# Kernel tuning notes

Measured on AMD Instinct MI355X. Metric: run time of the kernel, lower is better.

Reference implementation:

```python
import jax, jax.numpy as jnp
import numpy as np

EPS = 1e-5

def _layernorm(x, w, b):
    mu = jnp.mean(x, axis=-1, keepdims=True)
    var = jnp.mean(jnp.square(x - mu), axis=-1, keepdims=True)
    return (x - mu) * jax.lax.rsqrt(var + EPS) * w + b

def setup_inputs() -> dict:
    key = jax.random.key(0)
    ks = jax.random.split(key, 9)
    N, P_DIM, D = 16384, 3072, 1024
    patches = jax.random.normal(ks[0], (N, P_DIM), dtype=jnp.float32)
    bbox_coords = jax.random.uniform(ks[1], (N, 4), dtype=jnp.float32)
    ln1_w = jnp.ones((P_DIM,), dtype=jnp.float32)
    ln1_b = jnp.zeros((P_DIM,), dtype=jnp.float32)
    W_patch = jax.random.normal(ks[2], (D, P_DIM), dtype=jnp.float32) * (P_DIM ** -0.5)
    class_emb = jax.random.normal(ks[3], (1, 1, D), dtype=jnp.float32)
    W_pos = jax.random.normal(ks[4], (D, 4), dtype=jnp.float32) * 0.5
    b_pos = jax.random.normal(ks[5], (D,), dtype=jnp.float32) * 0.02
    class_pos = jax.random.normal(ks[6], (1, D), dtype=jnp.float32)
    return {"patches": patches, "bbox_coords": bbox_coords, "ln1_w": ln1_w,
            "ln1_b": ln1_b, "W_patch": W_patch, "class_emb": class_emb,
            "W_pos": W_pos, "b_pos": b_pos, "class_pos": class_pos}

def reference(patches, bbox_coords, ln1_w, ln1_b, W_patch, class_emb, W_pos, b_pos, class_pos):
    # Batched equivalent of the per-patch loop: LayerNorm -> Linear (no bias).
    # NOTE: torch code computes patch_norm2 but appends the PRE-norm2 embedding,
    # so norm2 is dead code and omitted here.
    x = _layernorm(patches, ln1_w, ln1_b)                      # [N, patch_dim]
    patch_embeds = jnp.einsum('np,dp->nd', x, W_patch)          # [N, D]
    embeddings = jnp.concatenate([class_emb, patch_embeds[None]], axis=1)  # [1, N+1, D]
    pos = jnp.einsum('nc,dc->nd', bbox_coords, W_pos) + b_pos   # [N, D]
    pos_full = jnp.concatenate([class_pos[None], pos[None]], axis=1)       # [1, N+1, D]
    return embeddings + pos_full
```

## Files before the change

kernel.cpp:

```cpp
#include <hip/hip_runtime.h>

typedef unsigned short u16;
typedef __attribute__((ext_vector_type(8))) short bf16x8;
typedef __attribute__((ext_vector_type(4))) float f32x4;

#define AS1C(p) ((const __attribute__((address_space(1))) void*)(p))
#define AS3(p)  ((__attribute__((address_space(3))) void*)(p))

__device__ __forceinline__ u16 f2bf(float f) {
    unsigned u = __float_as_uint(f);
    u += 0x7fffu + ((u >> 16) & 1u);
    return (u16)(u >> 16);
}

__global__ __launch_bounds__(256) void ln_cast_kernel(
    const float* __restrict__ x, const float* __restrict__ w,
    const float* __restrict__ b, u16* __restrict__ A, int K)
{
    const int row = blockIdx.x;
    const int t = threadIdx.x;
    const float* xr = x + (size_t)row * K;

    float4 v[3];
#pragma unroll
    for (int i = 0; i < 3; ++i)
        v[i] = *(const float4*)&xr[(i * 256 + t) * 4];

    float s = 0.f;
#pragma unroll
    for (int i = 0; i < 3; ++i) s += v[i].x + v[i].y + v[i].z + v[i].w;
#pragma unroll
    for (int off = 32; off; off >>= 1) s += __shfl_down(s, off);

    __shared__ float red[8];
    const int wid = t >> 6, lane = t & 63;
    if (lane == 0) red[wid] = s;
    __syncthreads();
    const float mu = (red[0] + red[1] + red[2] + red[3]) * (1.0f / 3072.0f);

    float sq = 0.f;
#pragma unroll
    for (int i = 0; i < 3; ++i) {
        float dx = v[i].x - mu, dy = v[i].y - mu, dz = v[i].z - mu, dw = v[i].w - mu;
        sq += dx * dx + dy * dy + dz * dz + dw * dw;
    }
#pragma unroll
    for (int off = 32; off; off >>= 1) sq += __shfl_down(sq, off);
    if (lane == 0) red[4 + wid] = sq;
    __syncthreads();
    const float var = (red[4] + red[5] + red[6] + red[7]) * (1.0f / 3072.0f);
    const float inv = rsqrtf(var + 1e-5f);

#pragma unroll
    for (int i = 0; i < 3; ++i) {
        const int j = (i * 256 + t) * 4;
        const float4 wv = *(const float4*)&w[j];
        const float4 bv = *(const float4*)&b[j];
        ushort4 o;
        o.x = f2bf((v[i].x - mu) * inv * wv.x + bv.x);
        o.y = f2bf((v[i].y - mu) * inv * wv.y + bv.y);
        o.z = f2bf((v[i].z - mu) * inv * wv.z + bv.z);
        o.w = f2bf((v[i].w - mu) * inv * wv.w + bv.w);
        *(ushort4*)&A[(size_t)row * K + j] = o;
    }
}

__global__ __launch_bounds__(256) void cast_w_kernel(
    const float* __restrict__ Wp, u16* __restrict__ Wb, int n4)
{
    const int i = blockIdx.x * 256 + threadIdx.x;
    if (i < n4) {
        const float4 v = ((const float4*)Wp)[i];
        ushort4 o;
        o.x = f2bf(v.x); o.y = f2bf(v.y); o.z = f2bf(v.z); o.w = f2bf(v.w);
        ((ushort4*)Wb)[i] = o;
    }
}

__global__ __launch_bounds__(256) void class_row_kernel(
    const float* __restrict__ ce, const float* __restrict__ cp,
    float* __restrict__ out, int D)
{
    const int i = blockIdx.x * 256 + threadIdx.x;
    if (i < D) out[i] = ce[i] + cp[i];
}

#define STG_A(BUFOFS, R0, T_) \
    __builtin_amdgcn_global_load_lds(AS1C(aS + (size_t)(R0) * 3072 + (T_) * 64), \
                                     AS3(dA + (BUFOFS) + (R0) * 128), 16, 0, 0)
#define STG_B(BUFOFS, R0, T_) \
    __builtin_amdgcn_global_load_lds(AS1C(bS + (size_t)(R0) * 3072 + (T_) * 64), \
                                     AS3(dB + (BUFOFS) + (R0) * 128), 16, 0, 0)

#define MFMA(d, a, b) d = __builtin_amdgcn_mfma_f32_16x16x32_bf16(a, b, d, 0, 0, 0)

#define PHASE(BUF, MH, CK, STG, WT) do {                                          \
    const char* Lb = L + (BUF);                                                   \
    bf16x8 a0 = *(const bf16x8*)(Lb + aRowBase + (MH)*8192 + 0*2048 + (CK));      \
    bf16x8 a1 = *(const bf16x8*)(Lb + aRowBase + (MH)*8192 + 1*2048 + (CK));      \
    bf16x8 a2 = *(const bf16x8*)(Lb + aRowBase + (MH)*8192 + 2*2048 + (CK));      \
    bf16x8 a3 = *(const bf16x8*)(Lb + aRowBase + (MH)*8192 + 3*2048 + (CK));      \
    bf16x8 b0 = *(const bf16x8*)(Lb + bRowBase + 0*2048 + (CK));                  \
    bf16x8 b1 = *(const bf16x8*)(Lb + bRowBase + 1*2048 + (CK));                  \
    bf16x8 b2 = *(const bf16x8*)(Lb + bRowBase + 2*2048 + (CK));                  \
    bf16x8 b3 = *(const bf16x8*)(Lb + bRowBase + 3*2048 + (CK));                  \
    STG;                                                                          \
    __builtin_amdgcn_s_barrier();                                                 \
    asm volatile("s_waitcnt lgkmcnt(0)" ::: "memory");                            \
    __builtin_amdgcn_s_setprio(1);                                                \
    MFMA(acc[(MH)*4+0][0], a0, b0); MFMA(acc[(MH)*4+0][1], a0, b1);               \
    MFMA(acc[(MH)*4+0][2], a0, b2); MFMA(acc[(MH)*4+0][3], a0, b3);               \
    MFMA(acc[(MH)*4+1][0], a1, b0); MFMA(acc[(MH)*4+1][1], a1, b1);               \
    MFMA(acc[(MH)*4+1][2], a1, b2); MFMA(acc[(MH)*4+1][3], a1, b3);               \
    MFMA(acc[(MH)*4+2][0], a2, b0); MFMA(acc[(MH)*4+2][1], a2, b1);               \
    MFMA(acc[(MH)*4+2][2], a2, b2); MFMA(acc[(MH)*4+2][3], a2, b3);               \
    MFMA(acc[(MH)*4+3][0], a3, b0); MFMA(acc[(MH)*4+3][1], a3, b1);               \
    MFMA(acc[(MH)*4+3][2], a3, b2); MFMA(acc[(MH)*4+3][3], a3, b3);               \
    __builtin_amdgcn_s_setprio(0);                                                \
    WT;                                                                           \
    __builtin_amdgcn_s_barrier();                                                 \
} while (0)

__global__ __launch_bounds__(512, 2) void gemm_256_8ph_kernel(
    const u16* __restrict__ A, const u16* __restrict__ W,
    const float* __restrict__ bbox, const float* __restrict__ Wpos,
    const float* __restrict__ bpos, float* __restrict__ out,
    int D)
{
    __shared__ __align__(16) char lds[131072];
    const char* L = (const char*)lds;
    const int K = 3072;
    const int NK = 48;

    const int bid = blockIdx.x;
    const int swb = (bid & 7) * 32 + (bid >> 3);
    const int bx = swb & 3;
    const int by = swb >> 2;
    const int brow = by * 256;
    const int bcol = bx * 256;

    const int t = threadIdx.x;
    const int wid = t >> 6, lane = t & 63;
    const int wm = wid >> 2;
    const int wn = wid & 3;
    const int fr = lane & 15;
    const int kq16 = ((lane >> 4) & 3) * 16;
    const int xorb = (fr & 7) << 4;
    const int aRowBase = (wm * 128 + fr) * 128;
    const int bRowBase = 32768 + (wn * 64 + fr) * 128;
    const int ck0 = kq16 ^ xorb;
    const int ck1 = (64 + kq16) ^ xorb;

    const int srow = t >> 3;
    const int scol = ((t & 7) ^ ((t >> 3) & 7)) * 8;
    const u16* aS = A + (size_t)(brow + srow) * K + scol;
    const u16* bS = W + (size_t)(bcol + srow) * K + scol;
    char* dA = (char*)lds + t * 16;
    char* dB = (char*)lds + 32768 + t * 16;

    f32x4 acc[8][4] = {};

    STG_A(0, 0, 0);   STG_A(0, 64, 0);  STG_A(0, 128, 0); STG_A(0, 192, 0);
    STG_B(0, 0, 0);   STG_B(0, 64, 0);  STG_B(0, 128, 0); STG_B(0, 192, 0);
    STG_A(65536, 0, 1); STG_A(65536, 128, 1);
    asm volatile("s_waitcnt vmcnt(2)" ::: "memory");
    __builtin_amdgcn_s_barrier();

    for (int T = 0; T < NK; T += 2) {
        const bool more = (T + 2) < NK;
        PHASE(0, 0, ck0, { STG_A(65536, 64, T + 1); STG_A(65536, 192, T + 1); }, ((void)0));
        PHASE(0, 1, ck0, { STG_B(65536, 0, T + 1); STG_B(65536, 64, T + 1); }, ((void)0));
        PHASE(0, 0, ck1, { STG_B(65536, 128, T + 1); STG_B(65536, 192, T + 1); }, ((void)0));
        PHASE(0, 1, ck1,
              { if (more) { STG_A(0, 0, T + 2); STG_A(0, 128, T + 2); } },
              { if (more) asm volatile("s_waitcnt vmcnt(2)" ::: "memory");
                else      asm volatile("s_waitcnt vmcnt(0)" ::: "memory"); });
        PHASE(65536, 0, ck0, { if (more) { STG_A(0, 64, T + 2); STG_A(0, 192, T + 2); } }, ((void)0));
        PHASE(65536, 1, ck0, { if (more) { STG_B(0, 0, T + 2); STG_B(0, 64, T + 2); } }, ((void)0));
        PHASE(65536, 0, ck1, { if (more) { STG_B(0, 128, T + 2); STG_B(0, 192, T + 2); } }, ((void)0));
        PHASE(65536, 1, ck1,
              { if (more) { STG_A(65536, 0, T + 3); STG_A(65536, 128, T + 3); } },
              { asm volatile("s_waitcnt vmcnt(2)" ::: "memory"); });
    }

    const int crow0 = brow + wm * 128 + ((lane >> 4) & 3) * 4;
    const int ccol = bcol + wn * 64 + fr;

    float4 wp[4];
    float bp[4];
#pragma unroll
    for (int n = 0; n < 4; ++n) {
        const int gc = ccol + n * 16;
        wp[n] = *(const float4*)&Wpos[gc * 4];
        bp[n] = bpos[gc];
    }

#pragma unroll
    for (int mi = 0; mi < 8; ++mi) {
#pragma unroll
        for (int r = 0; r < 4; ++r) {
            const int gr = crow0 + mi * 16 + r;
            const float4 bb = *(const float4*)&bbox[(size_t)gr * 4];
            float* orow = out + (size_t)(gr + 1) * D;
#pragma unroll
            for (int n = 0; n < 4; ++n) {
                const float pos = bp[n] + bb.x * wp[n].x + bb.y * wp[n].y
                                        + bb.z * wp[n].z + bb.w * wp[n].w;
                orow[ccol + n * 16] = acc[mi][n][r] + pos;
            }
        }
    }
}

extern "C" void kernel_launch(void* const* d_in, const int* in_sizes, int n_in,
                              void* d_out, int out_size, void* d_ws, size_t ws_size,
                              hipStream_t stream)
{
    const float* patches   = (const float*)d_in[0];
    const float* bbox      = (const float*)d_in[1];
    const float* ln1_w     = (const float*)d_in[2];
    const float* ln1_b     = (const float*)d_in[3];
    const float* W_patch   = (const float*)d_in[4];
    const float* class_emb = (const float*)d_in[5];
    const float* W_pos     = (const float*)d_in[6];
    const float* b_pos     = (const float*)d_in[7];
    const float* class_pos = (const float*)d_in[8];
    float* out = (float*)d_out;

    const int N = in_sizes[1] / 4;
    const int K = in_sizes[2];
    const int D = in_sizes[7];

    u16* Abf = (u16*)d_ws;
    u16* Wbf = Abf + (size_t)N * K;

    ln_cast_kernel<<<N, 256, 0, stream>>>(patches, ln1_w, ln1_b, Abf, K);

    const int n4 = (D * K) / 4;
    cast_w_kernel<<<(n4 + 255) / 256, 256, 0, stream>>>(W_patch, Wbf, n4);

    class_row_kernel<<<(D + 255) / 256, 256, 0, stream>>>(class_emb, class_pos, out, D);

    const int nblk = (N / 256) * (D / 256);
    gemm_256_8ph_kernel<<<nblk, 512, 0, stream>>>(Abf, Wbf, bbox, W_pos, b_pos, out, D);
}
```

Baseline: 158.3 us.

## Switch GEMM to 32x32x16 MFMA, stage epilogue through LDS, merge prep kernels

Replaces the 16x16x32 bf16 MFMA tiling with 32x32x16 MFMAs, so each wave issues fewer, larger matrix instructions per phase and reads fewer LDS fragments. The epilogue now writes accumulators to LDS and reads them back row-contiguous, so each lane emits float4 coalesced global stores with the positional bias fused in. The LayerNorm cast, weight cast and class-row kernels are merged into one launch to cut launch overhead. The cost is extra barriers and LDS traffic in the epilogue, plus a fragment layout mapping that must be exactly right for correctness.

```diff
diff --git a/kernel.cpp b/kernel.cpp
--- a/kernel.cpp
+++ b/kernel.cpp
@@ -2,7 +2,7 @@
 
 typedef unsigned short u16;
 typedef __attribute__((ext_vector_type(8))) short bf16x8;
-typedef __attribute__((ext_vector_type(4))) float f32x4;
+typedef __attribute__((ext_vector_type(16))) float f32x16;
 
 #define AS1C(p) ((const __attribute__((address_space(1))) void*)(p))
 #define AS3(p)  ((__attribute__((address_space(3))) void*)(p))
@@ -13,76 +13,78 @@
     return (u16)(u >> 16);
 }
 
-__global__ __launch_bounds__(256) void ln_cast_kernel(
+__global__ __launch_bounds__(256) void prep_kernel(
     const float* __restrict__ x, const float* __restrict__ w,
-    const float* __restrict__ b, u16* __restrict__ A, int K)
+    const float* __restrict__ b, const float* __restrict__ Wp,
+    const float* __restrict__ ce, const float* __restrict__ cp,
+    u16* __restrict__ A, u16* __restrict__ Wb, float* __restrict__ out,
+    int N, int D, int K)
 {
-    const int row = blockIdx.x;
+    const int blk = blockIdx.x;
     const int t = threadIdx.x;
-    const float* xr = x + (size_t)row * K;
-
-    float4 v[3];
-#pragma unroll
-    for (int i = 0; i < 3; ++i)
-        v[i] = *(const float4*)&xr[(i * 256 + t) * 4];
-
-    float s = 0.f;
-#pragma unroll
-    for (int i = 0; i < 3; ++i) s += v[i].x + v[i].y + v[i].z + v[i].w;
-#pragma unroll
-    for (int off = 32; off; off >>= 1) s += __shfl_down(s, off);
-
-    __shared__ float red[8];
-    const int wid = t >> 6, lane = t & 63;
-    if (lane == 0) red[wid] = s;
-    __syncthreads();
-    const float mu = (red[0] + red[1] + red[2] + red[3]) * (1.0f / 3072.0f);
-
-    float sq = 0.f;
-#pragma unroll
-    for (int i = 0; i < 3; ++i) {
-        float dx = v[i].x - mu, dy = v[i].y - mu, dz = v[i].z - mu, dw = v[i].w - mu;
-        sq += dx * dx + dy * dy + dz * dz + dw * dw;
-    }
-#pragma unroll
-    for (int off = 32; off; off >>= 1) sq += __shfl_down(sq, off);
-    if (lane == 0) red[4 + wid] = sq;
-    __syncthreads();
-    const float var = (red[4] + red[5] + red[6] + red[7]) * (1.0f / 3072.0f);
-    const float inv = rsqrtf(var + 1e-5f);
-
-#pragma unroll
-    for (int i = 0; i < 3; ++i) {
-        const int j = (i * 256 + t) * 4;
-        const float4 wv = *(const float4*)&w[j];
-        const float4 bv = *(const float4*)&b[j];
-        ushort4 o;
-        o.x = f2bf((v[i].x - mu) * inv * wv.x + bv.x);
-        o.y = f2bf((v[i].y - mu) * inv * wv.y + bv.y);
-        o.z = f2bf((v[i].z - mu) * inv * wv.z + bv.z);
-        o.w = f2bf((v[i].w - mu) * inv * wv.w + bv.w);
-        *(ushort4*)&A[(size_t)row * K + j] = o;
-    }
-}
-
-__global__ __launch_bounds__(256) void cast_w_kernel(
-    const float* __restrict__ Wp, u16* __restrict__ Wb, int n4)
-{
-    const int i = blockIdx.x * 256 + threadIdx.x;
-    if (i < n4) {
-        const float4 v = ((const float4*)Wp)[i];
-        ushort4 o;
-        o.x = f2bf(v.x); o.y = f2bf(v.y); o.z = f2bf(v.z); o.w = f2bf(v.w);
-        ((ushort4*)Wb)[i] = o;
-    }
-}
-
-__global__ __launch_bounds__(256) void class_row_kernel(
-    const float* __restrict__ ce, const float* __restrict__ cp,
-    float* __restrict__ out, int D)
-{
-    const int i = blockIdx.x * 256 + threadIdx.x;
-    if (i < D) out[i] = ce[i] + cp[i];
+
+    if (blk < N) {
+        const float* xr = x + (size_t)blk * K;
+        float4 v[3];
+#pragma unroll
+        for (int i = 0; i < 3; ++i)
+            v[i] = *(const float4*)&xr[(i * 256 + t) * 4];
+
+        float s = 0.f;
+#pragma unroll
+        for (int i = 0; i < 3; ++i) s += v[i].x + v[i].y + v[i].z + v[i].w;
+#pragma unroll
+        for (int off = 32; off; off >>= 1) s += __shfl_down(s, off);
+
+        __shared__ float red[8];
+        const int wid = t >> 6, lane = t & 63;
+        if (lane == 0) red[wid] = s;
+        __syncthreads();
+        const float mu = (red[0] + red[1] + red[2] + red[3]) * (1.0f / 3072.0f);
+
+        float sq = 0.f;
+#pragma unroll
+        for (int i = 0; i < 3; ++i) {
+            float dx = v[i].x - mu, dy = v[i].y - mu, dz = v[i].z - mu, dw = v[i].w - mu;
+            sq += dx * dx + dy * dy + dz * dz + dw * dw;
+        }
+#pragma unroll
+        for (int off = 32; off; off >>= 1) sq += __shfl_down(sq, off);
+        if (lane == 0) red[4 + wid] = sq;
+        __syncthreads();
+        const float var = (red[4] + red[5] + red[6] + red[7]) * (1.0f / 3072.0f);
+        const float inv = rsqrtf(var + 1e-5f);
+
+#pragma unroll
+        for (int i = 0; i < 3; ++i) {
+            const int j = (i * 256 + t) * 4;
+            const float4 wv = *(const float4*)&w[j];
+            const float4 bv = *(const float4*)&b[j];
+            ushort4 o;
+            o.x = f2bf((v[i].x - mu) * inv * wv.x + bv.x);
+            o.y = f2bf((v[i].y - mu) * inv * wv.y + bv.y);
+            o.z = f2bf((v[i].z - mu) * inv * wv.z + bv.z);
+            o.w = f2bf((v[i].w - mu) * inv * wv.w + bv.w);
+            *(ushort4*)&A[(size_t)blk * K + j] = o;
+        }
+    } else if (blk < N + D) {
+        const int row = blk - N;
+        const float* wr = Wp + (size_t)row * K;
+#pragma unroll
+        for (int i = 0; i < 3; ++i) {
+            const int j = (i * 256 + t) * 4;
+            const float4 v = *(const float4*)&wr[j];
+            ushort4 o;
+            o.x = f2bf(v.x); o.y = f2bf(v.y); o.z = f2bf(v.z); o.w = f2bf(v.w);
+            *(ushort4*)&Wb[(size_t)row * K + j] = o;
+        }
+    } else {
+#pragma unroll
+        for (int i = 0; i < 4; ++i) {
+            const int j = i * 256 + t;
+            out[j] = ce[j] + cp[j];
+        }
+    }
 }
 
 #define STG_A(BUFOFS, R0, T_) \
@@ -92,30 +94,26 @@
     __builtin_amdgcn_global_load_lds(AS1C(bS + (size_t)(R0) * 3072 + (T_) * 64), \
                                      AS3(dB + (BUFOFS) + (R0) * 128), 16, 0, 0)
 
-#define MFMA(d, a, b) d = __builtin_amdgcn_mfma_f32_16x16x32_bf16(a, b, d, 0, 0, 0)
-
-#define PHASE(BUF, MH, CK, STG, WT) do {                                          \
+#define MFMA32(d, a, b) d = __builtin_amdgcn_mfma_f32_32x32x16_bf16(a, b, d, 0, 0, 0)
+
+#define PHASE32(BUF, MH, CKA, CKB, STG, WT) do {                                  \
     const char* Lb = L + (BUF);                                                   \
-    bf16x8 a0 = *(const bf16x8*)(Lb + aRowBase + (MH)*8192 + 0*2048 + (CK));      \
-    bf16x8 a1 = *(const bf16x8*)(Lb + aRowBase + (MH)*8192 + 1*2048 + (CK));      \
-    bf16x8 a2 = *(const bf16x8*)(Lb + aRowBase + (MH)*8192 + 2*2048 + (CK));      \
-    bf16x8 a3 = *(const bf16x8*)(Lb + aRowBase + (MH)*8192 + 3*2048 + (CK));      \
-    bf16x8 b0 = *(const bf16x8*)(Lb + bRowBase + 0*2048 + (CK));                  \
-    bf16x8 b1 = *(const bf16x8*)(Lb + bRowBase + 1*2048 + (CK));                  \
-    bf16x8 b2 = *(const bf16x8*)(Lb + bRowBase + 2*2048 + (CK));                  \
-    bf16x8 b3 = *(const bf16x8*)(Lb + bRowBase + 3*2048 + (CK));                  \
+    bf16x8 a00 = *(const bf16x8*)(Lb + aRowBase + (MH)*8192 + 0    + (CKA));      \
+    bf16x8 a01 = *(const bf16x8*)(Lb + aRowBase + (MH)*8192 + 0    + (CKB));      \
+    bf16x8 a10 = *(const bf16x8*)(Lb + aRowBase + (MH)*8192 + 4096 + (CKA));      \
+    bf16x8 a11 = *(const bf16x8*)(Lb + aRowBase + (MH)*8192 + 4096 + (CKB));      \
+    bf16x8 b00 = *(const bf16x8*)(Lb + bRowBase + 0    + (CKA));                  \
+    bf16x8 b01 = *(const bf16x8*)(Lb + bRowBase + 0    + (CKB));                  \
+    bf16x8 b10 = *(const bf16x8*)(Lb + bRowBase + 4096 + (CKA));                  \
+    bf16x8 b11 = *(const bf16x8*)(Lb + bRowBase + 4096 + (CKB));                  \
     STG;                                                                          \
     __builtin_amdgcn_s_barrier();                                                 \
     asm volatile("s_waitcnt lgkmcnt(0)" ::: "memory");                            \
     __builtin_amdgcn_s_setprio(1);                                                \
-    MFMA(acc[(MH)*4+0][0], a0, b0); MFMA(acc[(MH)*4+0][1], a0, b1);               \
-    MFMA(acc[(MH)*4+0][2], a0, b2); MFMA(acc[(MH)*4+0][3], a0, b3);               \
-    MFMA(acc[(MH)*4+1][0], a1, b0); MFMA(acc[(MH)*4+1][1], a1, b1);               \
-    MFMA(acc[(MH)*4+1][2], a1, b2); MFMA(acc[(MH)*4+1][3], a1, b3);               \
-    MFMA(acc[(MH)*4+2][0], a2, b0); MFMA(acc[(MH)*4+2][1], a2, b1);               \
-    MFMA(acc[(MH)*4+2][2], a2, b2); MFMA(acc[(MH)*4+2][3], a2, b3);               \
-    MFMA(acc[(MH)*4+3][0], a3, b0); MFMA(acc[(MH)*4+3][1], a3, b1);               \
-    MFMA(acc[(MH)*4+3][2], a3, b2); MFMA(acc[(MH)*4+3][3], a3, b3);               \
+    MFMA32(acc[(MH)*2+0][0], a00, b00); MFMA32(acc[(MH)*2+0][1], a00, b10);       \
+    MFMA32(acc[(MH)*2+1][0], a10, b00); MFMA32(acc[(MH)*2+1][1], a10, b10);       \
+    MFMA32(acc[(MH)*2+0][0], a01, b01); MFMA32(acc[(MH)*2+0][1], a01, b11);       \
+    MFMA32(acc[(MH)*2+1][0], a11, b01); MFMA32(acc[(MH)*2+1][1], a11, b11);       \
     __builtin_amdgcn_s_setprio(0);                                                \
     WT;                                                                           \
     __builtin_amdgcn_s_barrier();                                                 \
@@ -143,13 +141,15 @@
     const int wid = t >> 6, lane = t & 63;
     const int wm = wid >> 2;
     const int wn = wid & 3;
-    const int fr = lane & 15;
-    const int kq16 = ((lane >> 4) & 3) * 16;
-    const int xorb = (fr & 7) << 4;
-    const int aRowBase = (wm * 128 + fr) * 128;
-    const int bRowBase = 32768 + (wn * 64 + fr) * 128;
-    const int ck0 = kq16 ^ xorb;
-    const int ck1 = (64 + kq16) ^ xorb;
+    const int l31 = lane & 31;
+    const int klane16 = (lane >> 5) * 16;
+    const int xorb = (lane & 7) << 4;
+    const int aRowBase = (wm * 128 + l31) * 128;
+    const int bRowBase = 32768 + (wn * 64 + l31) * 128;
+    const int ckA0 = (0  + klane16) ^ xorb;
+    const int ckB0 = (32 + klane16) ^ xorb;
+    const int ckA1 = (64 + klane16) ^ xorb;
+    const int ckB1 = (96 + klane16) ^ xorb;
 
     const int srow = t >> 3;
     const int scol = ((t & 7) ^ ((t >> 3) & 7)) * 8;
@@ -158,7 +158,7 @@
     char* dA = (char*)lds + t * 16;
     char* dB = (char*)lds + 32768 + t * 16;
 
-    f32x4 acc[8][4] = {};
+    f32x16 acc[4][2] = {};
 
     STG_A(0, 0, 0);   STG_A(0, 64, 0);  STG_A(0, 128, 0); STG_A(0, 192, 0);
     STG_B(0, 0, 0);   STG_B(0, 64, 0);  STG_B(0, 128, 0); STG_B(0, 192, 0);
@@ -168,46 +168,58 @@
 
     for (int T = 0; T < NK; T += 2) {
         const bool more = (T + 2) < NK;
-        PHASE(0, 0, ck0, { STG_A(65536, 64, T + 1); STG_A(65536, 192, T + 1); }, ((void)0));
-        PHASE(0, 1, ck0, { STG_B(65536, 0, T + 1); STG_B(65536, 64, T + 1); }, ((void)0));
-        PHASE(0, 0, ck1, { STG_B(65536, 128, T + 1); STG_B(65536, 192, T + 1); }, ((void)0));
-        PHASE(0, 1, ck1,
+        PHASE32(0, 0, ckA0, ckB0, { STG_A(65536, 64, T + 1); STG_A(65536, 192, T + 1); }, ((void)0));
+        PHASE32(0, 1, ckA0, ckB0, { STG_B(65536, 0, T + 1); STG_B(65536, 64, T + 1); }, ((void)0));
+        PHASE32(0, 0, ckA1, ckB1, { STG_B(65536, 128, T + 1); STG_B(65536, 192, T + 1); }, ((void)0));
+        PHASE32(0, 1, ckA1, ckB1,
               { if (more) { STG_A(0, 0, T + 2); STG_A(0, 128, T + 2); } },
               { if (more) asm volatile("s_waitcnt vmcnt(2)" ::: "memory");
                 else      asm volatile("s_waitcnt vmcnt(0)" ::: "memory"); });
-        PHASE(65536, 0, ck0, { if (more) { STG_A(0, 64, T + 2); STG_A(0, 192, T + 2); } }, ((void)0));
-        PHASE(65536, 1, ck0, { if (more) { STG_B(0, 0, T + 2); STG_B(0, 64, T + 2); } }, ((void)0));
-        PHASE(65536, 0, ck1, { if (more) { STG_B(0, 128, T + 2); STG_B(0, 192, T + 2); } }, ((void)0));
-        PHASE(65536, 1, ck1,
+        PHASE32(65536, 0, ckA0, ckB0, { if (more) { STG_A(0, 64, T + 2); STG_A(0, 192, T + 2); } }, ((void)0));
+        PHASE32(65536, 1, ckA0, ckB0, { if (more) { STG_B(0, 0, T + 2); STG_B(0, 64, T + 2); } }, ((void)0));
+        PHASE32(65536, 0, ckA1, ckB1, { if (more) { STG_B(0, 128, T + 2); STG_B(0, 192, T + 2); } }, ((void)0));
+        PHASE32(65536, 1, ckA1, ckB1,
               { if (more) { STG_A(65536, 0, T + 3); STG_A(65536, 128, T + 3); } },
               { asm volatile("s_waitcnt vmcnt(2)" ::: "memory"); });
     }
 
-    const int crow0 = brow + wm * 128 + ((lane >> 4) & 3) * 4;
-    const int ccol = bcol + wn * 64 + fr;
-
-    float4 wp[4];
-    float bp[4];
-#pragma unroll
-    for (int n = 0; n < 4; ++n) {
-        const int gc = ccol + n * 16;
-        wp[n] = *(const float4*)&Wpos[gc * 4];
-        bp[n] = bpos[gc];
-    }
-
-#pragma unroll
-    for (int mi = 0; mi < 8; ++mi) {
-#pragma unroll
-        for (int r = 0; r < 4; ++r) {
-            const int gr = crow0 + mi * 16 + r;
+    float* Lf = (float*)lds;
+    const int lrofs = (lane >> 5) * 4;
+    const int cg = bcol + lane * 4;
+
+    float4 wpv[4];
+    float bpv[4];
+#pragma unroll
+    for (int j = 0; j < 4; ++j) {
+        wpv[j] = *(const float4*)&Wpos[(cg + j) * 4];
+        bpv[j] = bpos[cg + j];
+    }
+
+#pragma unroll
+    for (int mb = 0; mb < 4; ++mb) {
+        __builtin_amdgcn_s_barrier();
+#pragma unroll
+        for (int nb = 0; nb < 2; ++nb) {
+            const int cc = wn * 64 + nb * 32 + l31;
+#pragma unroll
+            for (int reg = 0; reg < 16; ++reg) {
+                const int frow = (reg & 3) + 8 * (reg >> 2) + lrofs;
+                Lf[(wm * 32 + frow) * 256 + cc] = acc[mb][nb][reg];
+            }
+        }
+        __builtin_amdgcn_s_barrier();
+#pragma unroll
+        for (int i = 0; i < 8; ++i) {
+            const int lrow = wid + 8 * i;
+            const int gr = brow + (lrow >> 5) * 128 + mb * 32 + (lrow & 31);
+            const float4 v = *(const float4*)&Lf[lrow * 256 + lane * 4];
             const float4 bb = *(const float4*)&bbox[(size_t)gr * 4];
-            float* orow = out + (size_t)(gr + 1) * D;
-#pragma unroll
-            for (int n = 0; n < 4; ++n) {
-                const float pos = bp[n] + bb.x * wp[n].x + bb.y * wp[n].y
-                                        + bb.z * wp[n].z + bb.w * wp[n].w;
-                orow[ccol + n * 16] = acc[mi][n][r] + pos;
-            }
+            float4 o;
+            o.x = v.x + bpv[0] + bb.x * wpv[0].x + bb.y * wpv[0].y + bb.z * wpv[0].z + bb.w * wpv[0].w;
+            o.y = v.y + bpv[1] + bb.x * wpv[1].x + bb.y * wpv[1].y + bb.z * wpv[1].z + bb.w * wpv[1].w;
+            o.z = v.z + bpv[2] + bb.x * wpv[2].x + bb.y * wpv[2].y + bb.z * wpv[2].z + bb.w * wpv[2].w;
+            o.w = v.w + bpv[3] + bb.x * wpv[3].x + bb.y * wpv[3].y + bb.z * wpv[3].z + bb.w * wpv[3].w;
+            *(float4*)&out[(size_t)(gr + 1) * D + cg] = o;
         }
     }
 }
@@ -234,12 +246,9 @@
     u16* Abf = (u16*)d_ws;
     u16* Wbf = Abf + (size_t)N * K;
 
-    ln_cast_kernel<<<N, 256, 0, stream>>>(patches, ln1_w, ln1_b, Abf, K);
-
-    const int n4 = (D * K) / 4;
-    cast_w_kernel<<<(n4 + 255) / 256, 256, 0, stream>>>(W_patch, Wbf, n4);
-
-    class_row_kernel<<<(D + 255) / 256, 256, 0, stream>>>(class_emb, class_pos, out, D);
+    prep_kernel<<<N + D + 1, 256, 0, stream>>>(patches, ln1_w, ln1_b, W_patch,
+                                               class_emb, class_pos, Abf, Wbf, out,
+                                               N, D, K);
 
     const int nblk = (N / 256) * (D / 256);
     gemm_256_8ph_kernel<<<nblk, 512, 0, stream>>>(Abf, Wbf, bbox, W_pos, b_pos, out, D);
```

Result: slower. 168.9 us (+6.7%).
